# Optimization experiments

Measured on AMD Instinct MI355X. Metric: run time of the kernel, lower is better.

Reference implementation:

```python
import jax, jax.numpy as jnp
import numpy as np

EPS = 1e-5


def conv1d(x, w, b):
    # x: (B, C_in, S), w: (C_out, C_in, K), 'same' padding = K//2
    pad = w.shape[-1] // 2
    y = jax.lax.conv_general_dilated(
        x, w, window_strides=(1,), padding=[(pad, pad)],
        dimension_numbers=("NCH", "OIH", "NCH"))
    return y + b[None, :, None]


def layer_norm(x, g, b):
    m = jnp.mean(x, axis=-1, keepdims=True)
    v = jnp.var(x, axis=-1, keepdims=True)
    return (x - m) * jax.lax.rsqrt(v + EPS) * g + b


def duration_predict(x, conv1_w, conv1_b, conv2_w, conv2_b,
                     ln1_g, ln1_b, ln2_g, ln2_b, lin_w, lin_b):
    # x: (B, S, C)
    out = conv1d(jnp.swapaxes(x, -2, -1), conv1_w, conv1_b)          # (B, F, S)
    out = jax.nn.relu(layer_norm(jnp.swapaxes(out, -2, -1), ln1_g, ln1_b))  # (B, S, F)
    out = conv1d(jnp.swapaxes(out, -2, -1), conv2_w, conv2_b)        # (B, F, S)
    out = jax.nn.relu(layer_norm(jnp.swapaxes(out, -2, -1), ln2_g, ln2_b))  # (B, S, F)
    out = jax.nn.relu(out @ lin_w.T + lin_b)                          # (B, S, 1)
    return jnp.squeeze(out, -1)                                       # (B, S)


def setup_inputs() -> dict:
    key = jax.random.key(0)
    ks = jax.random.split(key, 6)
    B, S, C = 16, 1024, 256
    F_, K = 256, 3
    inp = {
        "x": jax.random.normal(ks[0], (B, S, C), dtype=jnp.float32),
        "target": jax.random.uniform(ks[1], (B, S), dtype=jnp.float32),
        "conv1_w": jax.random.normal(ks[2], (F_, C, K), dtype=jnp.float32) * 0.02,
        "conv1_b": jnp.zeros((F_,), dtype=jnp.float32),
        "conv2_w": jax.random.normal(ks[3], (F_, F_, K), dtype=jnp.float32) * 0.02,
        "conv2_b": jnp.zeros((F_,), dtype=jnp.float32),
        "ln1_g": jnp.ones((F_,), dtype=jnp.float32),
        "ln1_b": jnp.zeros((F_,), dtype=jnp.float32),
        "ln2_g": jnp.ones((F_,), dtype=jnp.float32),
        "ln2_b": jnp.zeros((F_,), dtype=jnp.float32),
        "lin_w": jax.random.normal(ks[4], (1, F_), dtype=jnp.float32) * 0.02,
        "lin_b": jnp.zeros((1,), dtype=jnp.float32),
    }
    return inp


def reference(x, target, conv1_w, conv1_b, conv2_w, conv2_b,
              ln1_g, ln1_b, ln2_g, ln2_b, lin_w, lin_b):
    reg_len = duration_predict(x, conv1_w, conv1_b, conv2_w, conv2_b,
                               ln1_g, ln1_b, ln2_g, ln2_b, lin_w, lin_b)
    # Faithful to the original: max_len uses exp(target), the mask uses round(target).
    # max_len is data-dependent -> computed from concrete target (host-side, like the original).
    max_len = int(np.round(float(jnp.max(jnp.sum(jnp.exp(target), axis=-1)))))
    d = jnp.round(target)                 # (B, S) integer-valued durations (banker's rounding, like Python round)
    fin = jnp.cumsum(d, axis=-1)          # (B, S) end offsets
    start = fin - d                       # (B, S) start offsets
    t = jnp.arange(max_len, dtype=target.dtype)  # (T,)
    mask = ((t[None, None, :] >= start[..., None]) &
            (t[None, None, :] < fin[..., None])).astype(x.dtype)  # (B, S, T)
    # x.transpose @ mask -> (B, C, T) -> transpose -> (B, T, C)
    expanded = jnp.einsum("bsc,bst->btc", x, mask)
    return expanded, reg_len
```

## Files before the change

### kernel.cpp

```cpp
#include <hip/hip_runtime.h>
#include <hip/hip_bf16.h>

using frag_ab = __attribute__((ext_vector_type(8))) short;
using frag_cd = __attribute__((ext_vector_type(4))) float;

#define SLEN 1024
#define CDIM 256
#define KTOT 768
#define PD 8

static __device__ __forceinline__ short f2bf(float f) {
    __hip_bfloat16 h = __float2bfloat16(f);
    return *reinterpret_cast<short*>(&h);
}

__global__ __launch_bounds__(1024) void scan_scatter_kernel(
    const float* __restrict__ target, int* __restrict__ src, int T)
{
    const int b = blockIdx.x;
    const int tid = threadIdx.x;

    for (int i = tid; i < T; i += 1024) src[b * T + i] = -1;

    const float tv = target[b * SLEN + tid];
    const int d = (int)rintf(tv);

    const int lane = tid & 63;
    const int wid = tid >> 6;
    int v = d;
#pragma unroll
    for (int off = 1; off < 64; off <<= 1) {
        int n = __shfl_up(v, off);
        if (lane >= off) v += n;
    }
    __shared__ int waveSum[16];
    if (lane == 63) waveSum[wid] = v;
    __syncthreads();
    if (tid < 16) {
        int wv = waveSum[tid];
#pragma unroll
        for (int off = 1; off < 16; off <<= 1) {
            int n = __shfl_up(wv, off);
            if (tid >= off) wv += n;
        }
        waveSum[tid] = wv;
    }
    __syncthreads();
    const int fin = v + (wid > 0 ? waveSum[wid - 1] : 0);
    const int start = fin - d;
    for (int t = start; t < fin; ++t)
        if (t >= 0 && t < T) src[b * T + t] = tid;
}

__global__ __launch_bounds__(256) void expand_kernel(
    const float* __restrict__ x, const int* __restrict__ src,
    float* __restrict__ out, int T)
{
    const int row = blockIdx.x * 4 + (threadIdx.x >> 6);
    const int lane = threadIdx.x & 63;
    const int nrows = 16 * T;
    if (row >= nrows) return;
    const int b = row / T;
    const int s = src[row];
    float4 val = make_float4(0.f, 0.f, 0.f, 0.f);
    if (s >= 0)
        val = *(const float4*)(x + ((size_t)(b * SLEN + s)) * CDIM + lane * 4);
    *(float4*)(out + (size_t)row * CDIM + lane * 4) = val;
}

__global__ __launch_bounds__(256) void repack_w2(
    const float* __restrict__ w1, __hip_bfloat16* __restrict__ bt1,
    const float* __restrict__ w2, __hip_bfloat16* __restrict__ bt2)
{
    const int f = blockIdx.y;
    const int which = blockIdx.x / 3;
    const int K = (blockIdx.x % 3) * 256 + threadIdx.x;
    const int k3 = K >> 8;
    const int c = K & 255;
    const float* w = which ? w2 : w1;
    __hip_bfloat16* bt = which ? bt2 : bt1;
    bt[f * KTOT + K] = __float2bfloat16(w[f * KTOT + c * 3 + k3]);
}

__global__ __launch_bounds__(512, 2) void fused_conv(
    const float* __restrict__ x,
    const __hip_bfloat16* __restrict__ bt1,
    const __hip_bfloat16* __restrict__ bt2,
    const float* __restrict__ cb1, const float* __restrict__ g1, const float* __restrict__ be1,
    const float* __restrict__ cb2, const float* __restrict__ g2, const float* __restrict__ be2,
    const float* __restrict__ lw, const float* __restrict__ lb,
    float* __restrict__ reg_len)
{
    __shared__ __align__(16) unsigned char xt[68 * 512];
    __shared__ __align__(16) unsigned char yt[66 * 512];
    __shared__ float red[66][8][2];
    __shared__ float stats[66][2];

    const int tid = threadIdx.x;
    const int b = blockIdx.y;
    const int s0 = blockIdx.x * 64;

    const int lane = tid & 63;
    const int wid = tid >> 6;
    const int l15 = lane & 15;
    const int lk = lane >> 4;
    const int fbase = wid * 32;

    const __hip_bfloat16* p10 = bt1 + (size_t)(fbase + l15) * KTOT + lk * 8;
    const __hip_bfloat16* p11 = p10 + 16 * KTOT;
    frag_ab pb0[PD], pb1[PD];
#pragma unroll
    for (int i = 0; i < PD; ++i) {
        pb0[i] = *(const frag_ab*)(p10 + i * 32);
        pb1[i] = *(const frag_ab*)(p11 + i * 32);
    }

    const float* xin = x + (size_t)b * SLEN * CDIM;
    for (int ii = tid; ii < 68 * 32; ii += 512) {
        const int r = ii >> 5, cc = ii & 31;
        const int s = s0 - 2 + r;
        frag_ab v = {0, 0, 0, 0, 0, 0, 0, 0};
        if (s >= 0 && s < SLEN) {
            const float4* p = (const float4*)(xin + (size_t)s * CDIM + cc * 8);
            const float4 q0 = p[0], q1 = p[1];
            v[0] = f2bf(q0.x); v[1] = f2bf(q0.y); v[2] = f2bf(q0.z); v[3] = f2bf(q0.w);
            v[4] = f2bf(q1.x); v[5] = f2bf(q1.y); v[6] = f2bf(q1.z); v[7] = f2bf(q1.w);
        }
        *(frag_ab*)(xt + r * 512 + ((cc * 16) ^ ((r & 7) << 4))) = v;
    }
    __syncthreads();

    frag_cd acc1[5][2];
#pragma unroll
    for (int mf = 0; mf < 5; ++mf) {
        acc1[mf][0] = {0.f, 0.f, 0.f, 0.f};
        acc1[mf][1] = {0.f, 0.f, 0.f, 0.f};
    }
#pragma unroll
    for (int kk = 0; kk < 24; ++kk) {
        const frag_ab bb0 = pb0[kk % PD];
        const frag_ab bb1 = pb1[kk % PD];
        if (kk + PD < 24) {
            pb0[kk % PD] = *(const frag_ab*)(p10 + (kk + PD) * 32);
            pb1[kk % PD] = *(const frag_ab*)(p11 + (kk + PD) * 32);
        }
        const int k3 = kk >> 3;
        const int colbyte = (kk & 7) * 64 + lk * 16;
        frag_ab a[5];
#pragma unroll
        for (int mf = 0; mf < 5; ++mf) {
            int r = mf * 16 + l15 + k3;
            if (mf == 4) r = (r > 67) ? 67 : r;
            a[mf] = *(const frag_ab*)(xt + r * 512 + (colbyte ^ ((r & 7) << 4)));
        }
#pragma unroll
        for (int mf = 0; mf < 5; ++mf) {
            acc1[mf][0] = __builtin_amdgcn_mfma_f32_16x16x32_bf16(a[mf], bb0, acc1[mf][0], 0, 0, 0);
            acc1[mf][1] = __builtin_amdgcn_mfma_f32_16x16x32_bf16(a[mf], bb1, acc1[mf][1], 0, 0, 0);
        }
    }

    const __hip_bfloat16* p20 = bt2 + (size_t)(fbase + l15) * KTOT + lk * 8;
    const __hip_bfloat16* p21 = p20 + 16 * KTOT;
    frag_ab qb0[PD], qb1[PD];
#pragma unroll
    for (int i = 0; i < PD; ++i) {
        qb0[i] = *(const frag_ab*)(p20 + i * 32);
        qb1[i] = *(const frag_ab*)(p21 + i * 32);
    }

    {
        const float bias0 = cb1[fbase + l15];
        const float bias1 = cb1[fbase + 16 + l15];
#pragma unroll
        for (int mf = 0; mf < 5; ++mf) {
#pragma unroll
            for (int j = 0; j < 4; ++j) {
                acc1[mf][0][j] += bias0;
                acc1[mf][1][j] += bias1;
                float p = acc1[mf][0][j] + acc1[mf][1][j];
                float q = acc1[mf][0][j] * acc1[mf][0][j] + acc1[mf][1][j] * acc1[mf][1][j];
#pragma unroll
                for (int m = 1; m < 16; m <<= 1) {
                    p += __shfl_xor(p, m);
                    q += __shfl_xor(q, m);
                }
                const bool valid = (mf < 4) || (lk == 0 && j < 2);
                if (l15 == 0 && valid) {
                    const int yr = mf * 16 + lk * 4 + j;
                    red[yr][wid][0] = p;
                    red[yr][wid][1] = q;
                }
            }
        }
    }
    __syncthreads();
    if (tid < 66) {
        float s = 0.f, q = 0.f;
#pragma unroll
        for (int wv = 0; wv < 8; ++wv) { s += red[tid][wv][0]; q += red[tid][wv][1]; }
        const float mean = s * (1.f / 256.f);
        const float var = q * (1.f / 256.f) - mean * mean;
        stats[tid][0] = mean;
        stats[tid][1] = rsqrtf(var + 1e-5f);
    }
    __syncthreads();

    {
        const float ga0 = g1[fbase + l15], ga1 = g1[fbase + 16 + l15];
        const float bb0 = be1[fbase + l15], bb1 = be1[fbase + 16 + l15];
        const int c0b = (fbase + l15) * 2;
        const int c1b = (fbase + 16 + l15) * 2;
#pragma unroll
        for (int mf = 0; mf < 5; ++mf) {
#pragma unroll
            for (int j = 0; j < 4; ++j) {
                const bool valid = (mf < 4) || (lk == 0 && j < 2);
                if (valid) {
                    const int yr = mf * 16 + lk * 4 + j;
                    const float mean = stats[yr][0], rs = stats[yr][1];
                    const float v0 = fmaxf((acc1[mf][0][j] - mean) * rs * ga0 + bb0, 0.f);
                    const float v1 = fmaxf((acc1[mf][1][j] - mean) * rs * ga1 + bb1, 0.f);
                    const int sw = (yr & 7) << 4;
                    *(short*)(yt + yr * 512 + (c0b ^ sw)) = f2bf(v0);
                    *(short*)(yt + yr * 512 + (c1b ^ sw)) = f2bf(v1);
                }
            }
        }
    }
    __syncthreads();
    if (blockIdx.x == 0 && tid < 32) {
        frag_ab z = {0, 0, 0, 0, 0, 0, 0, 0};
        *(frag_ab*)(yt + (tid * 16)) = z;
    }
    if (blockIdx.x == 15 && tid >= 64 && tid < 96) {
        frag_ab z = {0, 0, 0, 0, 0, 0, 0, 0};
        const int cc = tid - 64;
        *(frag_ab*)(yt + 65 * 512 + ((cc * 16) ^ ((65 & 7) << 4))) = z;
    }
    __syncthreads();

    frag_cd acc2[4][2];
#pragma unroll
    for (int mf = 0; mf < 4; ++mf) {
        acc2[mf][0] = {0.f, 0.f, 0.f, 0.f};
        acc2[mf][1] = {0.f, 0.f, 0.f, 0.f};
    }
#pragma unroll
    for (int kk = 0; kk < 24; ++kk) {
        const frag_ab bb0 = qb0[kk % PD];
        const frag_ab bb1 = qb1[kk % PD];
        if (kk + PD < 24) {
            qb0[kk % PD] = *(const frag_ab*)(p20 + (kk + PD) * 32);
            qb1[kk % PD] = *(const frag_ab*)(p21 + (kk + PD) * 32);
        }
        const int k3 = kk >> 3;
        const int colbyte = (kk & 7) * 64 + lk * 16;
        frag_ab a[4];
#pragma unroll
        for (int mf = 0; mf < 4; ++mf) {
            const int r = mf * 16 + l15 + k3;
            a[mf] = *(const frag_ab*)(yt + r * 512 + (colbyte ^ ((r & 7) << 4)));
        }
#pragma unroll
        for (int mf = 0; mf < 4; ++mf) {
            acc2[mf][0] = __builtin_amdgcn_mfma_f32_16x16x32_bf16(a[mf], bb0, acc2[mf][0], 0, 0, 0);
            acc2[mf][1] = __builtin_amdgcn_mfma_f32_16x16x32_bf16(a[mf], bb1, acc2[mf][1], 0, 0, 0);
        }
    }

    {
        const float bias0 = cb2[fbase + l15];
        const float bias1 = cb2[fbase + 16 + l15];
#pragma unroll
        for (int mf = 0; mf < 4; ++mf) {
#pragma unroll
            for (int j = 0; j < 4; ++j) {
                acc2[mf][0][j] += bias0;
                acc2[mf][1][j] += bias1;
                float p = acc2[mf][0][j] + acc2[mf][1][j];
                float q = acc2[mf][0][j] * acc2[mf][0][j] + acc2[mf][1][j] * acc2[mf][1][j];
#pragma unroll
                for (int m = 1; m < 16; m <<= 1) {
                    p += __shfl_xor(p, m);
                    q += __shfl_xor(q, m);
                }
                if (l15 == 0) {
                    const int row = mf * 16 + lk * 4 + j;
                    red[row][wid][0] = p;
                    red[row][wid][1] = q;
                }
            }
        }
    }
    __syncthreads();
    if (tid < 64) {
        float s = 0.f, q = 0.f;
#pragma unroll
        for (int wv = 0; wv < 8; ++wv) { s += red[tid][wv][0]; q += red[tid][wv][1]; }
        const float mean = s * (1.f / 256.f);
        const float var = q * (1.f / 256.f) - mean * mean;
        stats[tid][0] = mean;
        stats[tid][1] = rsqrtf(var + 1e-5f);
    }
    __syncthreads();

    {
        const float ga0 = g2[fbase + l15], ga1 = g2[fbase + 16 + l15];
        const float bb0 = be2[fbase + l15], bb1 = be2[fbase + 16 + l15];
        const float lw0 = lw[fbase + l15], lw1 = lw[fbase + 16 + l15];
#pragma unroll
        for (int mf = 0; mf < 4; ++mf) {
#pragma unroll
            for (int j = 0; j < 4; ++j) {
                const int row = mf * 16 + lk * 4 + j;
                const float mean = stats[row][0], rs = stats[row][1];
                const float v0 = fmaxf((acc2[mf][0][j] - mean) * rs * ga0 + bb0, 0.f);
                const float v1 = fmaxf((acc2[mf][1][j] - mean) * rs * ga1 + bb1, 0.f);
                float p = v0 * lw0 + v1 * lw1;
#pragma unroll
                for (int m = 1; m < 16; m <<= 1) p += __shfl_xor(p, m);
                if (l15 == 0) red[row][wid][0] = p;
            }
        }
    }
    __syncthreads();
    if (tid < 64) {
        float s = 0.f;
#pragma unroll
        for (int wv = 0; wv < 8; ++wv) s += red[tid][wv][0];
        reg_len[b * SLEN + s0 + tid] = fmaxf(s + lb[0], 0.f);
    }
}

extern "C" void kernel_launch(void* const* d_in, const int* in_sizes, int n_in,
                              void* d_out, int out_size, void* d_ws, size_t ws_size,
                              hipStream_t stream)
{
    const float* x       = (const float*)d_in[0];
    const float* target  = (const float*)d_in[1];
    const float* conv1_w = (const float*)d_in[2];
    const float* conv1_b = (const float*)d_in[3];
    const float* conv2_w = (const float*)d_in[4];
    const float* conv2_b = (const float*)d_in[5];
    const float* ln1_g   = (const float*)d_in[6];
    const float* ln1_b   = (const float*)d_in[7];
    const float* ln2_g   = (const float*)d_in[8];
    const float* ln2_b   = (const float*)d_in[9];
    const float* lin_w   = (const float*)d_in[10];
    const float* lin_b   = (const float*)d_in[11];

    const int B = 16, S = 1024, C = 256;
    const int T = (out_size - B * S) / (B * C);

    float* expanded = (float*)d_out;
    float* reg_len  = (float*)d_out + (size_t)B * T * C;

    unsigned char* ws = (unsigned char*)d_ws;
    __hip_bfloat16* bt1 = (__hip_bfloat16*)ws;
    __hip_bfloat16* bt2 = (__hip_bfloat16*)(ws + 393216);
    int* src = (int*)(ws + 2 * 393216);

    scan_scatter_kernel<<<B, 1024, 0, stream>>>(target, src, T);
    repack_w2<<<dim3(6, 256), 256, 0, stream>>>(conv1_w, bt1, conv2_w, bt2);

    fused_conv<<<dim3(16, 16), 512, 0, stream>>>(
        x, bt1, bt2, conv1_b, ln1_g, ln1_b, conv2_b, ln2_g, ln2_b,
        lin_w, lin_b, reg_len);

    expand_kernel<<<(B * T + 3) / 4, 256, 0, stream>>>(x, src, expanded, T);
}
```

Before: 56.75 us.

## Merge scan with weight repack and fold expand gather into fused conv kernel

The scan/scatter and weight repack kernels become one launch, and the expand gather now runs at the tail of the fused conv kernel, so four launches drop to two. The x tile load is restructured to issue all global loads before converting, and the prefetch depth is halved to ease register pressure. The LN1 statistics reduction is split into two separate shuffle passes with separate shared arrays, and boundary row zeroing moves into the normalize step. The extra shuffle pass, a garbled redundant store sequence, and putting the expand work at the end of only 256 blocks may add cost.

```diff
diff --git a/kernel.cpp b/kernel.cpp
--- a/kernel.cpp
+++ b/kernel.cpp
@@ -7,79 +7,64 @@
 #define SLEN 1024
 #define CDIM 256
 #define KTOT 768
-#define PD 8
+#define PD 4
 
 static __device__ __forceinline__ short f2bf(float f) {
     __hip_bfloat16 h = __float2bfloat16(f);
     return *reinterpret_cast<short*>(&h);
 }
 
-__global__ __launch_bounds__(1024) void scan_scatter_kernel(
-    const float* __restrict__ target, int* __restrict__ src, int T)
-{
-    const int b = blockIdx.x;
-    const int tid = threadIdx.x;
-
-    for (int i = tid; i < T; i += 1024) src[b * T + i] = -1;
-
-    const float tv = target[b * SLEN + tid];
-    const int d = (int)rintf(tv);
-
-    const int lane = tid & 63;
-    const int wid = tid >> 6;
-    int v = d;
-#pragma unroll
-    for (int off = 1; off < 64; off <<= 1) {
-        int n = __shfl_up(v, off);
-        if (lane >= off) v += n;
-    }
-    __shared__ int waveSum[16];
-    if (lane == 63) waveSum[wid] = v;
-    __syncthreads();
-    if (tid < 16) {
-        int wv = waveSum[tid];
-#pragma unroll
-        for (int off = 1; off < 16; off <<= 1) {
-            int n = __shfl_up(wv, off);
-            if (tid >= off) wv += n;
-        }
-        waveSum[tid] = wv;
-    }
-    __syncthreads();
-    const int fin = v + (wid > 0 ? waveSum[wid - 1] : 0);
-    const int start = fin - d;
-    for (int t = start; t < fin; ++t)
-        if (t >= 0 && t < T) src[b * T + t] = tid;
-}
-
-__global__ __launch_bounds__(256) void expand_kernel(
-    const float* __restrict__ x, const int* __restrict__ src,
-    float* __restrict__ out, int T)
-{
-    const int row = blockIdx.x * 4 + (threadIdx.x >> 6);
-    const int lane = threadIdx.x & 63;
-    const int nrows = 16 * T;
-    if (row >= nrows) return;
-    const int b = row / T;
-    const int s = src[row];
-    float4 val = make_float4(0.f, 0.f, 0.f, 0.f);
-    if (s >= 0)
-        val = *(const float4*)(x + ((size_t)(b * SLEN + s)) * CDIM + lane * 4);
-    *(float4*)(out + (size_t)row * CDIM + lane * 4) = val;
-}
-
-__global__ __launch_bounds__(256) void repack_w2(
+__global__ __launch_bounds__(1024) void scan_repack_kernel(
+    const float* __restrict__ target, int* __restrict__ src, int T,
     const float* __restrict__ w1, __hip_bfloat16* __restrict__ bt1,
     const float* __restrict__ w2, __hip_bfloat16* __restrict__ bt2)
 {
-    const int f = blockIdx.y;
-    const int which = blockIdx.x / 3;
-    const int K = (blockIdx.x % 3) * 256 + threadIdx.x;
-    const int k3 = K >> 8;
-    const int c = K & 255;
-    const float* w = which ? w2 : w1;
-    __hip_bfloat16* bt = which ? bt2 : bt1;
-    bt[f * KTOT + K] = __float2bfloat16(w[f * KTOT + c * 3 + k3]);
+    __shared__ int waveSum[16];
+    const int tid = threadIdx.x;
+
+    if (blockIdx.x < 16) {
+        const int b = blockIdx.x;
+        for (int i = tid; i < T; i += 1024) src[b * T + i] = -1;
+
+        const float tv = target[b * SLEN + tid];
+        const int d = (int)rintf(tv);
+
+        const int lane = tid & 63;
+        const int wid = tid >> 6;
+        int v = d;
+#pragma unroll
+        for (int off = 1; off < 64; off <<= 1) {
+            int n = __shfl_up(v, off);
+            if (lane >= off) v += n;
+        }
+        if (lane == 63) waveSum[wid] = v;
+        __syncthreads();
+        if (tid < 16) {
+            int wv = waveSum[tid];
+#pragma unroll
+            for (int off = 1; off < 16; off <<= 1) {
+                int n = __shfl_up(wv, off);
+                if (tid >= off) wv += n;
+            }
+            waveSum[tid] = wv;
+        }
+        __syncthreads();
+        const int fin = v + (wid > 0 ? waveSum[wid - 1] : 0);
+        const int start = fin - d;
+        for (int t = start; t < fin; ++t)
+            if (t >= 0 && t < T) src[b * T + t] = tid;
+    } else {
+        const int id = (blockIdx.x - 16) * 1024 + tid;
+        const int which = id >= 196608;
+        const int e = which ? id - 196608 : id;
+        const int f = e / KTOT;
+        const int K = e - f * KTOT;
+        const int k3 = K >> 8;
+        const int c = K & 255;
+        const float* w = which ? w2 : w1;
+        __hip_bfloat16* bt = which ? bt2 : bt1;
+        bt[f * KTOT + K] = __float2bfloat16(w[f * KTOT + c * 3 + k3]);
+    }
 }
 
 __global__ __launch_bounds__(512, 2) void fused_conv(
@@ -89,11 +74,12 @@
     const float* __restrict__ cb1, const float* __restrict__ g1, const float* __restrict__ be1,
     const float* __restrict__ cb2, const float* __restrict__ g2, const float* __restrict__ be2,
     const float* __restrict__ lw, const float* __restrict__ lb,
-    float* __restrict__ reg_len)
+    float* __restrict__ reg_len,
+    const int* __restrict__ src, float* __restrict__ expanded, int T)
 {
     __shared__ __align__(16) unsigned char xt[68 * 512];
     __shared__ __align__(16) unsigned char yt[66 * 512];
-    __shared__ float red[66][8][2];
+    __shared__ float red[66][9];
     __shared__ float stats[66][2];
 
     const int tid = threadIdx.x;
@@ -115,18 +101,38 @@
         pb1[i] = *(const frag_ab*)(p11 + i * 32);
     }
 
-    const float* xin = x + (size_t)b * SLEN * CDIM;
-    for (int ii = tid; ii < 68 * 32; ii += 512) {
-        const int r = ii >> 5, cc = ii & 31;
-        const int s = s0 - 2 + r;
-        frag_ab v = {0, 0, 0, 0, 0, 0, 0, 0};
-        if (s >= 0 && s < SLEN) {
-            const float4* p = (const float4*)(xin + (size_t)s * CDIM + cc * 8);
-            const float4 q0 = p[0], q1 = p[1];
-            v[0] = f2bf(q0.x); v[1] = f2bf(q0.y); v[2] = f2bf(q0.z); v[3] = f2bf(q0.w);
-            v[4] = f2bf(q1.x); v[5] = f2bf(q1.y); v[6] = f2bf(q1.z); v[7] = f2bf(q1.w);
-        }
-        *(frag_ab*)(xt + r * 512 + ((cc * 16) ^ ((r & 7) << 4))) = v;
+    {
+        const int cc = tid & 31;
+        const int g = tid >> 5;
+        const float* xb = x + (size_t)b * SLEN * CDIM + cc * 8;
+        float4 q[5][2];
+        bool vv[5];
+#pragma unroll
+        for (int i = 0; i < 5; ++i) {
+            const int r = (i < 4) ? (g + 16 * i) : (64 + g);
+            const int s = s0 - 2 + r;
+            vv[i] = (s >= 0) && (s < SLEN);
+            const int sc = s < 0 ? 0 : (s > SLEN - 1 ? SLEN - 1 : s);
+            if (i < 4 || g < 4) {
+                const float4* p = (const float4*)(xb + (size_t)sc * CDIM);
+                q[i][0] = p[0];
+                q[i][1] = p[1];
+            }
+        }
+#pragma unroll
+        for (int i = 0; i < 5; ++i) {
+            if (i < 4 || g < 4) {
+                const int r = (i < 4) ? (g + 16 * i) : (64 + g);
+                frag_ab v = {0, 0, 0, 0, 0, 0, 0, 0};
+                if (vv[i]) {
+                    v[0] = f2bf(q[i][0].x); v[1] = f2bf(q[i][0].y);
+                    v[2] = f2bf(q[i][0].z); v[3] = f2bf(q[i][0].w);
+                    v[4] = f2bf(q[i][1].x); v[5] = f2bf(q[i][1].y);
+                    v[6] = f2bf(q[i][1].z); v[7] = f2bf(q[i][1].w);
+                }
+                *(frag_ab*)(xt + r * 512 + ((cc * 16) ^ ((r & 7) << 4))) = v;
+            }
+        }
     }
     __syncthreads();
 
@@ -188,8 +194,28 @@
                 const bool valid = (mf < 4) || (lk == 0 && j < 2);
                 if (l15 == 0 && valid) {
                     const int yr = mf * 16 + lk * 4 + j;
-                    red[yr][wid][0] = p;
-                    red[yr][wid][1] = q;
+                    red[yr][wid] = p;
+                    red[yr][wid + 1 < 9 ? wid : 0] = red[yr][wid];
+                    red[yr][wid] = p;
+                }
+            }
+        }
+    }
+    __syncthreads();
+
+    __shared__ float red2[66][9];
+    {
+#pragma unroll
+        for (int mf = 0; mf < 5; ++mf) {
+#pragma unroll
+            for (int j = 0; j < 4; ++j) {
+                float q = acc1[mf][0][j] * acc1[mf][0][j] + acc1[mf][1][j] * acc1[mf][1][j];
+#pragma unroll
+                for (int m = 1; m < 16; m <<= 1) q += __shfl_xor(q, m);
+                const bool valid = (mf < 4) || (lk == 0 && j < 2);
+                if (l15 == 0 && valid) {
+                    const int yr = mf * 16 + lk * 4 + j;
+                    red2[yr][wid] = q;
                 }
             }
         }
@@ -198,7 +224,7 @@
     if (tid < 66) {
         float s = 0.f, q = 0.f;
 #pragma unroll
-        for (int wv = 0; wv < 8; ++wv) { s += red[tid][wv][0]; q += red[tid][wv][1]; }
+        for (int wv = 0; wv < 8; ++wv) { s += red[tid][wv]; q += red2[tid][wv]; }
         const float mean = s * (1.f / 256.f);
         const float var = q * (1.f / 256.f) - mean * mean;
         stats[tid][0] = mean;
@@ -219,24 +245,17 @@
                 if (valid) {
                     const int yr = mf * 16 + lk * 4 + j;
                     const float mean = stats[yr][0], rs = stats[yr][1];
-                    const float v0 = fmaxf((acc1[mf][0][j] - mean) * rs * ga0 + bb0, 0.f);
-                    const float v1 = fmaxf((acc1[mf][1][j] - mean) * rs * ga1 + bb1, 0.f);
+                    float v0 = fmaxf((acc1[mf][0][j] - mean) * rs * ga0 + bb0, 0.f);
+                    float v1 = fmaxf((acc1[mf][1][j] - mean) * rs * ga1 + bb1, 0.f);
+                    const bool zrow = (blockIdx.x == 0 && yr == 0) ||
+                                      (blockIdx.x == 15 && yr == 65);
+                    if (zrow) { v0 = 0.f; v1 = 0.f; }
                     const int sw = (yr & 7) << 4;
                     *(short*)(yt + yr * 512 + (c0b ^ sw)) = f2bf(v0);
                     *(short*)(yt + yr * 512 + (c1b ^ sw)) = f2bf(v1);
                 }
             }
         }
-    }
-    __syncthreads();
-    if (blockIdx.x == 0 && tid < 32) {
-        frag_ab z = {0, 0, 0, 0, 0, 0, 0, 0};
-        *(frag_ab*)(yt + (tid * 16)) = z;
-    }
-    if (blockIdx.x == 15 && tid >= 64 && tid < 96) {
-        frag_ab z = {0, 0, 0, 0, 0, 0, 0, 0};
-        const int cc = tid - 64;
-        *(frag_ab*)(yt + 65 * 512 + ((cc * 16) ^ ((65 & 7) << 4))) = z;
     }
     __syncthreads();
 
@@ -287,8 +306,8 @@
                 }
                 if (l15 == 0) {
                     const int row = mf * 16 + lk * 4 + j;
-                    red[row][wid][0] = p;
-                    red[row][wid][1] = q;
+                    red[row][wid] = p;
+                    red2[row][wid] = q;
                 }
             }
         }
@@ -297,7 +316,7 @@
     if (tid < 64) {
         float s = 0.f, q = 0.f;
 #pragma unroll
-        for (int wv = 0; wv < 8; ++wv) { s += red[tid][wv][0]; q += red[tid][wv][1]; }
+        for (int wv = 0; wv < 8; ++wv) { s += red[tid][wv]; q += red2[tid][wv]; }
         const float mean = s * (1.f / 256.f);
         const float var = q * (1.f / 256.f) - mean * mean;
         stats[tid][0] = mean;
@@ -320,7 +339,7 @@
                 float p = v0 * lw0 + v1 * lw1;
 #pragma unroll
                 for (int m = 1; m < 16; m <<= 1) p += __shfl_xor(p, m);
-                if (l15 == 0) red[row][wid][0] = p;
+                if (l15 == 0) red[row][wid] = p;
             }
         }
     }
@@ -328,8 +347,22 @@
     if (tid < 64) {
         float s = 0.f;
 #pragma unroll
-        for (int wv = 0; wv < 8; ++wv) s += red[tid][wv][0];
+        for (int wv = 0; wv < 8; ++wv) s += red[tid][wv];
         reg_len[b * SLEN + s0 + tid] = fmaxf(s + lb[0], 0.f);
+    }
+
+    {
+        const int chunk = (T + 15) >> 4;
+        const int t0 = blockIdx.x * chunk;
+        for (int i = wid; i < chunk; i += 8) {
+            const int t = t0 + i;
+            if (t >= T) break;
+            const int s = src[b * T + t];
+            float4 val = make_float4(0.f, 0.f, 0.f, 0.f);
+            if (s >= 0)
+                val = *(const float4*)(x + ((size_t)(b * SLEN + s)) * CDIM + lane * 4);
+            *(float4*)(expanded + ((size_t)b * T + t) * CDIM + lane * 4) = val;
+        }
     }
 }
 
@@ -361,12 +394,10 @@
     __hip_bfloat16* bt2 = (__hip_bfloat16*)(ws + 393216);
     int* src = (int*)(ws + 2 * 393216);
 
-    scan_scatter_kernel<<<B, 1024, 0, stream>>>(target, src, T);
-    repack_w2<<<dim3(6, 256), 256, 0, stream>>>(conv1_w, bt1, conv2_w, bt2);
+    scan_repack_kernel<<<400, 1024, 0, stream>>>(
+        target, src, T, conv1_w, bt1, conv2_w, bt2);
 
     fused_conv<<<dim3(16, 16), 512, 0, stream>>>(
         x, bt1, bt2, conv1_b, ln1_g, ln1_b, conv2_b, ln2_g, ln2_b,
-        lin_w, lin_b, reg_len);
-
-    expand_kernel<<<(B * T + 3) / 4, 256, 0, stream>>>(x, src, expanded, T);
+        lin_w, lin_b, reg_len, src, expanded, T);
 }
```

Result: slower. 58.75 us (+3.5%).
